# Performance work log

Measured on AMD Instinct MI355X. Metric: run time of the kernel, lower is better.

## Reference

```python
import jax, jax.numpy as jnp
import numpy as np

B, L, D, H = 2, 2048, 1024, 16
HD = D // H
ROPE_BASE = 10000.0


def _chain_info(lengths):
    """lengths: [B, L] int, chain lengths packed at the front, zeros after.
    Returns per-position within-chain positions (RoPE resets per chain),
    chain ids, and a validity mask."""
    def one(row):
        csum = jnp.cumsum(row)                      # [L]
        total = csum[-1]
        p = jnp.arange(L)
        cid = jnp.searchsorted(csum, p, side='right')  # chain id per position
        prev = jnp.where(cid > 0, csum[jnp.clip(cid - 1, 0, L - 1)], 0)
        valid = p < total
        pos = jnp.where(valid, p - prev, 0).astype(jnp.float32)
        return pos, cid, valid
    return jax.vmap(one)(lengths)


def _rope_tables(pos):
    # pos: [B, L] float -> cos/sin [B, L, 1, HD]
    inv_freq = 1.0 / (ROPE_BASE ** (jnp.arange(0, HD, 2, dtype=jnp.float32) / HD))
    freqs = pos[..., None] * inv_freq               # [B, L, HD/2]
    emb = jnp.concatenate([freqs, freqs], axis=-1)  # [B, L, HD]
    return jnp.cos(emb)[:, :, None, :], jnp.sin(emb)[:, :, None, :]


def _apply_rope(x, cos, sin):
    d = x.shape[-1]
    x1, x2 = x[..., : d // 2], x[..., d // 2:]
    return x * cos + jnp.concatenate([-x2, x1], axis=-1) * sin


def _branch(x, Wqkv, bqkv, cos, sin, allowed):
    # x: [B, L, D]; allowed: [B, L, L] bool attention mask for this branch
    qkv = x @ Wqkv.T + bqkv                          # [B, L, 3D]
    qkv = qkv.reshape(B, L, 3, H, HD)
    q, k, v = qkv[:, :, 0], qkv[:, :, 1], qkv[:, :, 2]
    q = q * (HD ** -0.5)
    q = _apply_rope(q, cos, sin)
    k = _apply_rope(k, cos, sin)
    scores = jnp.einsum('bthd,bshd->bhts', q, k)     # [B, H, L, L]
    scores = jnp.where(allowed[:, None], scores, -jnp.inf)
    probs = jax.nn.softmax(scores, axis=-1)
    probs = jnp.where(jnp.isnan(probs), 0.0, probs)  # fully-masked rows -> 0
    out = jnp.einsum('bhts,bshd->bthd', probs, v)    # [B, L, H, HD]
    return out.reshape(B, L, D)


def setup_inputs() -> dict:
    key = jax.random.key(0)
    ks = jax.random.split(key, 7)
    s = 0.02
    lens = np.zeros((B, L), np.int64)
    lens[0, :8] = [300, 250, 200, 400, 350, 248, 150, 100]   # sum 1998
    lens[1, :6] = [512, 400, 300, 360, 276, 200]             # sum 2048
    return {
        'hidden_states': jax.random.normal(ks[0], (B, L, D), jnp.float32),
        'attention_mask_in_length': jnp.asarray(lens),
        'Wqkv_intra': jax.random.normal(ks[1], (3 * D, D), jnp.float32) * s,
        'bqkv_intra': jnp.zeros((3 * D,), jnp.float32),
        'Wqkv_inter': jax.random.normal(ks[2], (3 * D, D), jnp.float32) * s,
        'bqkv_inter': jnp.zeros((3 * D,), jnp.float32),
        'Wout': jax.random.normal(ks[3], (D, D), jnp.float32) * s,
        'bout': jnp.zeros((D,), jnp.float32),
    }


def reference(hidden_states, attention_mask_in_length, Wqkv_intra, bqkv_intra,
              Wqkv_inter, bqkv_inter, Wout, bout):
    pos, cid, valid = _chain_info(attention_mask_in_length)
    cos, sin = _rope_tables(pos)
    same_chain = cid[:, :, None] == cid[:, None, :]          # [B, L, L]
    key_valid = valid[:, None, :]                            # [B, 1, L]
    allowed_intra = same_chain & key_valid
    allowed_inter = (~same_chain) & key_valid
    out_intra = _branch(hidden_states, Wqkv_intra, bqkv_intra, cos, sin, allowed_intra)
    out_inter = _branch(hidden_states, Wqkv_inter, bqkv_inter, cos, sin, allowed_inter)
    return (out_intra + out_inter) @ Wout.T + bout
```

## Files before the change

### kernel.cpp

```cpp
#include <hip/hip_runtime.h>
#include <hip/hip_bf16.h>
#include <stdint.h>

#define B 2
#define L 2048
#define D 1024
#define H 16
#define HD 64
#define NT (L / 64)
#define NQT (L / 128)
#define INVALID_CID 0x40000000
#define BHLHD ((size_t)B * H * L * HD)

typedef __hip_bfloat16 bf16;
typedef __attribute__((ext_vector_type(8))) short short8;
typedef __attribute__((ext_vector_type(4))) float floatx4;
typedef __attribute__((ext_vector_type(4))) unsigned int uint4v;

static __device__ __forceinline__ short f2bf(float f) {
    bf16 h = __float2bfloat16(f);
    return *reinterpret_cast<short*>(&h);
}

static __device__ __forceinline__ void async_copy16(const void* g, void* l) {
    __builtin_amdgcn_global_load_lds((__attribute__((address_space(1))) void*)g,
                                     (__attribute__((address_space(3))) void*)l,
                                     16, 0, 0);
}

__global__ void chain_kernel(const int* __restrict__ lens,
                             float* __restrict__ pos, int* __restrict__ cid,
                             int4* __restrict__ tinfo)
{
    __shared__ int csum[L];
    __shared__ int cids[L];
    __shared__ int part[256];
    int b = blockIdx.x;
    int t = threadIdx.x;

    int loc[8];
    int s = 0;
    #pragma unroll
    for (int j = 0; j < 8; ++j) { s += lens[b * L + t * 8 + j]; loc[j] = s; }
    part[t] = s;
    __syncthreads();
    if (t == 0) {
        int acc = 0;
        for (int i = 0; i < 256; ++i) { int v = part[i]; part[i] = acc; acc += v; }
    }
    __syncthreads();
    int base = part[t];
    #pragma unroll
    for (int j = 0; j < 8; ++j) csum[t * 8 + j] = base + loc[j];
    __syncthreads();

    int total = csum[L - 1];
    for (int p = t; p < L; p += 256) {
        int cv;
        if (p < total) {
            int lo = 0, hi = L;
            while (lo < hi) {
                int mid = (lo + hi) >> 1;
                if (csum[mid] <= p) lo = mid + 1; else hi = mid;
            }
            int prev = (lo > 0) ? csum[lo - 1] : 0;
            pos[b * L + p] = (float)(p - prev);
            cv = lo;
        } else {
            pos[b * L + p] = 0.f;
            cv = INVALID_CID;
        }
        cids[p] = cv;
        cid[b * L + p] = cv;
    }
    __syncthreads();
    if (t < NT) {
        int mn = 0x7fffffff, mx = -1, any = 0, all = 1;
        for (int j = 0; j < 64; ++j) {
            int cv = cids[t * 64 + j];
            if (cv != INVALID_CID) { any = 1; mn = min(mn, cv); mx = max(mx, cv); }
            else all = 0;
        }
        tinfo[b * NT + t] = make_int4(mn, mx, any | (all << 1), 0);
    }
}

__global__ void rope_table(const float* __restrict__ pos, float2* __restrict__ tab)
{
    int idx = blockIdx.x * 256 + threadIdx.x;
    int j = idx & 31, l = idx >> 5;
    float invf = exp2f(-(float)j * (13.287712379549449f / 32.f));
    float ang = pos[l] * invf;
    tab[idx] = make_float2(cosf(ang), sinf(ang));
}

__global__ void cast_all(const float* __restrict__ x,  const float* __restrict__ Wi,
                         const float* __restrict__ We, const float* __restrict__ Wo,
                         bf16* __restrict__ xb, bf16* __restrict__ Wib,
                         bf16* __restrict__ Web, bf16* __restrict__ Wob)
{
    int bid = blockIdx.x;
    const float* src; bf16* dst; int base;
    if      (bid < 4096)  { src = x;  dst = xb;  base = bid; }
    else if (bid < 7168)  { src = Wi; dst = Wib; base = bid - 4096; }
    else if (bid < 10240) { src = We; dst = Web; base = bid - 7168; }
    else                  { src = Wo; dst = Wob; base = bid - 10240; }
    int i = (base * 256 + threadIdx.x) * 4;
    float4 v = *(const float4*)(src + i);
    dst[i + 0] = __float2bfloat16(v.x);
    dst[i + 1] = __float2bfloat16(v.y);
    dst[i + 2] = __float2bfloat16(v.z);
    dst[i + 3] = __float2bfloat16(v.w);
}

__global__ __launch_bounds__(256, 4) void gemm_qkv(
    const bf16* __restrict__ A, const bf16* __restrict__ Bw,
    const float* __restrict__ bi, const float* __restrict__ be,
    const float2* __restrict__ tab,
    bf16* __restrict__ Qo, bf16* __restrict__ Ko, bf16* __restrict__ Vto)
{
    __shared__ short Smem[2 * 128 * 32];
    short* As = Smem;
    short* Bs = Smem + 128 * 32;

    int tid = threadIdx.x;
    int wave = tid >> 6, lane = tid & 63;
    int i15 = lane & 15, q8 = lane >> 4;
    int wm = wave & 1, wn = wave >> 1;
    int m0 = blockIdx.y * 128, n0 = blockIdx.x * 128;
    const int K = D;

    floatx4 acc[4][4];
    #pragma unroll
    for (int mt = 0; mt < 4; ++mt)
        #pragma unroll
        for (int nt = 0; nt < 4; ++nt) acc[mt][nt] = (floatx4){0.f, 0.f, 0.f, 0.f};

    const short* gA = (const short*)A  + (size_t)(m0 + wave * 32 + (lane >> 2)) * K + (lane & 3) * 8;
    const short* gB = (const short*)Bw + (size_t)(n0 + wave * 32 + (lane >> 2)) * K + (lane & 3) * 8;
    short* lA = As + wave * 1024;
    short* lB = Bs + wave * 1024;

    for (int kt = 0; kt < K; kt += 32) {
        __syncthreads();
        async_copy16(gA + kt,          lA);
        async_copy16(gA + 16 * K + kt, lA + 512);
        async_copy16(gB + kt,          lB);
        async_copy16(gB + 16 * K + kt, lB + 512);
        __syncthreads();

        short8 af[4], bfr[4];
        #pragma unroll
        for (int mt = 0; mt < 4; ++mt)
            af[mt] = *(const short8*)&As[(wm * 64 + mt * 16 + i15) * 32 + q8 * 8];
        #pragma unroll
        for (int nt = 0; nt < 4; ++nt)
            bfr[nt] = *(const short8*)&Bs[(wn * 64 + nt * 16 + i15) * 32 + q8 * 8];
        #pragma unroll
        for (int mt = 0; mt < 4; ++mt)
            #pragma unroll
            for (int nt = 0; nt < 4; ++nt)
                acc[mt][nt] = __builtin_amdgcn_mfma_f32_16x16x32_bf16(af[mt], bfr[nt], acc[mt][nt], 0, 0, 0);
    }

    int nb = n0 + wn * 64;
    int segw = nb >> 10;
    int br = (segw >= 3);
    int st = segw - 3 * br;
    int h = (nb >> 6) & (H - 1);
    int b = m0 >> 11;
    int lb = (m0 & (L - 1)) + wm * 64;

    float bv[4];
    #pragma unroll
    for (int nt = 0; nt < 4; ++nt) {
        int n = nb + nt * 16 + i15;
        bv[nt] = (n < 3 * D) ? bi[n] : be[n - 3 * D];
    }

    if (st != 2) {
        bf16* out = (st == 0 ? Qo : Ko) + (size_t)br * BHLHD;
        const size_t bh = (size_t)(b * H + h) * L;
        float qs = (st == 0) ? 0.18033688011111772f : 1.0f;
        #pragma unroll
        for (int mt = 0; mt < 4; ++mt) {
            #pragma unroll
            for (int rg = 0; rg < 4; ++rg) {
                int m = m0 + wm * 64 + mt * 16 + q8 * 4 + rg;
                int l = lb + mt * 16 + q8 * 4 + rg;
                float2 cs0 = tab[(size_t)m * 32 + i15];
                float2 cs1 = tab[(size_t)m * 32 + 16 + i15];
                size_t orow = (bh + l) * HD;
                #pragma unroll
                for (int nt = 0; nt < 4; ++nt) {
                    float x  = acc[mt][nt][rg] + bv[nt];
                    float pr = acc[mt][nt ^ 2][rg] + bv[nt ^ 2];
                    float cc = (nt & 1) ? cs1.x : cs0.x;
                    float ss = (nt & 1) ? cs1.y : cs0.y;
                    float v = qs * (x * cc + ((nt < 2) ? -pr : pr) * ss);
                    out[orow + nt * 16 + i15] = __float2bfloat16(v);
                }
            }
        }
    } else {
        bf16* out = Vto + (size_t)br * BHLHD;
        const size_t bhd = (size_t)(b * H + h) * HD;
        __syncthreads();
        short* vts = Smem + wave * 64 * 20;
        #pragma unroll
        for (int mt = 0; mt < 4; ++mt) {
            #pragma unroll
            for (int nt = 0; nt < 4; ++nt) {
                uint2 w;
                w.x = (unsigned)(unsigned short)f2bf(acc[mt][nt][0] + bv[nt]) |
                      ((unsigned)(unsigned short)f2bf(acc[mt][nt][1] + bv[nt]) << 16);
                w.y = (unsigned)(unsigned short)f2bf(acc[mt][nt][2] + bv[nt]) |
                      ((unsigned)(unsigned short)f2bf(acc[mt][nt][3] + bv[nt]) << 16);
                *(uint2*)&vts[(nt * 16 + i15) * 20 + q8 * 4] = w;
            }
            uint2 r0 = *(const uint2*)&vts[lane * 20 + 0];
            uint2 r1 = *(const uint2*)&vts[lane * 20 + 4];
            uint2 r2 = *(const uint2*)&vts[lane * 20 + 8];
            uint2 r3 = *(const uint2*)&vts[lane * 20 + 12];
            size_t ga = (bhd + lane) * L + lb + mt * 16;
            uint4v v0 = (uint4v){r0.x, r0.y, r1.x, r1.y};
            uint4v v1 = (uint4v){r2.x, r2.y, r3.x, r3.y};
            *(uint4v*)&out[ga]     = v0;
            *(uint4v*)&out[ga + 8] = v1;
        }
    }
}

__global__ __launch_bounds__(256, 4) void gemm128(
    const bf16* __restrict__ A, const bf16* __restrict__ Bw,
    const float* __restrict__ bias, void* __restrict__ Cout,
    int M, int N, int K, int c_bf16)
{
    __shared__ short As[128 * 32];
    __shared__ short Bs[128 * 32];

    int tid = threadIdx.x;
    int wave = tid >> 6, lane = tid & 63;
    int i15 = lane & 15, q8 = lane >> 4;
    int wm = wave & 1, wn = wave >> 1;
    int m0 = blockIdx.y * 128, n0 = blockIdx.x * 128;

    floatx4 acc[4][4];
    #pragma unroll
    for (int mt = 0; mt < 4; ++mt)
        #pragma unroll
        for (int nt = 0; nt < 4; ++nt) acc[mt][nt] = (floatx4){0.f, 0.f, 0.f, 0.f};

    const short* gA = (const short*)A  + (size_t)(m0 + wave * 32 + (lane >> 2)) * K + (lane & 3) * 8;
    const short* gB = (const short*)Bw + (size_t)(n0 + wave * 32 + (lane >> 2)) * K + (lane & 3) * 8;
    short* lA = As + wave * 1024;
    short* lB = Bs + wave * 1024;

    for (int kt = 0; kt < K; kt += 32) {
        __syncthreads();
        async_copy16(gA + kt,          lA);
        async_copy16(gA + 16 * K + kt, lA + 512);
        async_copy16(gB + kt,          lB);
        async_copy16(gB + 16 * K + kt, lB + 512);
        __syncthreads();

        short8 af[4], bfr[4];
        #pragma unroll
        for (int mt = 0; mt < 4; ++mt)
            af[mt] = *(const short8*)&As[(wm * 64 + mt * 16 + i15) * 32 + q8 * 8];
        #pragma unroll
        for (int nt = 0; nt < 4; ++nt)
            bfr[nt] = *(const short8*)&Bs[(wn * 64 + nt * 16 + i15) * 32 + q8 * 8];
        #pragma unroll
        for (int mt = 0; mt < 4; ++mt)
            #pragma unroll
            for (int nt = 0; nt < 4; ++nt)
                acc[mt][nt] = __builtin_amdgcn_mfma_f32_16x16x32_bf16(af[mt], bfr[nt], acc[mt][nt], 0, 0, 0);
    }

    #pragma unroll
    for (int nt = 0; nt < 4; ++nt) {
        int n = n0 + wn * 64 + nt * 16 + i15;
        float bv = bias[n];
        #pragma unroll
        for (int mt = 0; mt < 4; ++mt) {
            #pragma unroll
            for (int rg = 0; rg < 4; ++rg) {
                int m = m0 + wm * 64 + mt * 16 + q8 * 4 + rg;
                float v = acc[mt][nt][rg] + bv;
                if (c_bf16) ((bf16*)Cout)[(size_t)m * N + n] = __float2bfloat16(v);
                else        ((float*)Cout)[(size_t)m * N + n] = v;
            }
        }
    }
}

__global__ __launch_bounds__(256, 2) void attn6(
    const bf16* __restrict__ Q, const bf16* __restrict__ Kg, const bf16* __restrict__ Vtg,
    const int* __restrict__ cid, const int4* __restrict__ tinfo,
    float* __restrict__ OutF, bf16* __restrict__ OutB, const float* __restrict__ Prev,
    int branch)
{
    __shared__ short Ks[2][64][72];
    __shared__ short Vs[2][64][72];
    __shared__ int cls_s[NT];
    __shared__ int list_s[NT];
    __shared__ int nlist_s;

    int tid = threadIdx.x;
    int wave = tid >> 6, lane = tid & 63;
    int i15 = lane & 15, q8 = lane >> 4;
    int workid = ((blockIdx.x & 7) << 6) | (blockIdx.x >> 3);
    int qt = workid & (NQT - 1);
    int h  = (workid >> 4) & (H - 1);
    int b  = workid >> 8;
    int q0 = qt * 128;
    const size_t bh  = (size_t)(b * H + h) * L;
    const size_t bhd = (size_t)(b * H + h) * HD;

    short8 qf[2][2];
    int cq[2];
    #pragma unroll
    for (int g = 0; g < 2; ++g) {
        const short* qp = (const short*)Q + (bh + q0 + g * 64 + wave * 16 + i15) * HD + q8 * 8;
        qf[g][0] = *(const short8*)(qp);
        qf[g][1] = *(const short8*)(qp + 32);
        cq[g] = cid[b * L + q0 + g * 64 + wave * 16 + i15];
    }

    int4 qa = tinfo[b * NT + 2 * qt];
    int4 qb4 = tinfo[b * NT + 2 * qt + 1];
    int4 qinf;
    qinf.x = min(qa.x, qb4.x);
    qinf.y = max(qa.y, qb4.y);
    qinf.z = ((qa.z | qb4.z) & 1) | (qa.z & qb4.z & 2);
    int qall = (qinf.z >> 1) & 1;

    if (tid < NT) {
        int4 ki = tinfo[b * NT + tid];
        int kany = ki.z & 1, kall = (ki.z >> 1) & 1;
        bool disjoint = (ki.x > qinf.y) || (ki.y < qinf.x);
        bool mono = qall && kall && (qinf.x == qinf.y) && (ki.x == ki.y) && (qinf.x == ki.x);
        int cls;
        if (branch == 0) {
            if (!kany || disjoint) cls = 0;
            else if (mono) cls = 2;
            else cls = 1;
        } else {
            if (!kany || mono) cls = 0;
            else if (kall && disjoint) cls = 2;
            else cls = 1;
        }
        cls_s[tid] = cls;
    }
    __syncthreads();
    if (tid == 0) {
        int n = 0;
        for (int t = 0; t < NT; ++t) {
            int c = cls_s[t];
            if (c) list_s[n++] = (t * 64) | ((c == 2) << 16);
        }
        nlist_s = n;
    }
    __syncthreads();
    int n = nlist_s;

    int r = tid >> 2, ccol = (tid & 3) * 16;
    int sr = ((((r >> 2) & 1) | ((r >> 5) << 1)) << 4) | (((r >> 3) & 3) << 2) | (r & 3);
    const short* Kbase = (const short*)Kg  + (bh + r) * HD + ccol;
    const short* Vbase = (const short*)Vtg + (bhd + r) * L + ccol;

    int4 pk0, pk1, pv0, pv1;
    int cur = 0;
    if (n > 0) {
        cur = list_s[0];
        int kt0 = cur & 0xffff;
        pk0 = *(const int4*)(Kbase + (size_t)kt0 * HD);
        pk1 = *(const int4*)(Kbase + (size_t)kt0 * HD + 8);
        pv0 = *(const int4*)(Vbase + kt0);
        pv1 = *(const int4*)(Vbase + kt0 + 8);
    }

    floatx4 accO[2][4];
    #pragma unroll
    for (int g = 0; g < 2; ++g)
        #pragma unroll
        for (int t = 0; t < 4; ++t) accO[g][t] = (floatx4){0.f, 0.f, 0.f, 0.f};
    float lsum[2] = {0.f, 0.f};

    for (int i = 0; i < n; ++i) {
        int kt = cur & 0xffff, full = cur >> 16;
        int buf = i & 1;

        *(int4*)&Ks[buf][sr][ccol]     = pk0;
        *(int4*)&Ks[buf][sr][ccol + 8] = pk1;
        *(int4*)&Vs[buf][r][ccol]      = pv0;
        *(int4*)&Vs[buf][r][ccol + 8]  = pv1;
        __syncthreads();

        if (i + 1 < n) {
            cur = list_s[i + 1];
            int nk = cur & 0xffff;
            pk0 = *(const int4*)(Kbase + (size_t)nk * HD);
            pk1 = *(const int4*)(Kbase + (size_t)nk * HD + 8);
            pv0 = *(const int4*)(Vbase + nk);
            pv1 = *(const int4*)(Vbase + nk + 8);
        }

        unsigned int dl[2][4], dh[2][4];
        #pragma unroll
        for (int t = 0; t < 4; ++t) {
            short8 b0 = *(const short8*)&Ks[buf][t * 16 + i15][q8 * 8];
            short8 b1 = *(const short8*)&Ks[buf][t * 16 + i15][32 + q8 * 8];

            floatx4 accS[2];
            #pragma unroll
            for (int g = 0; g < 2; ++g) {
                accS[g] = (floatx4){0.f, 0.f, 0.f, 0.f};
                accS[g] = __builtin_amdgcn_mfma_f32_16x16x32_bf16(b0, qf[g][0], accS[g], 0, 0, 0);
                accS[g] = __builtin_amdgcn_mfma_f32_16x16x32_bf16(b1, qf[g][1], accS[g], 0, 0, 0);
            }

            if (!full) {
                int4 ck4 = *(const int4*)(cid + b * L + kt + (q8 << 3) + ((t & 1) << 2) + ((t >> 1) << 5));
                int ckr[4] = {ck4.x, ck4.y, ck4.z, ck4.w};
                #pragma unroll
                for (int g = 0; g < 2; ++g)
                    #pragma unroll
                    for (int rg = 0; rg < 4; ++rg) {
                        bool kv = (ckr[rg] != INVALID_CID);
                        bool match = (cq[g] == ckr[rg]);
                        bool ok = kv && (branch ? !match : match);
                        accS[g][rg] = ok ? accS[g][rg] : -1e30f;
                    }
            }

            #pragma unroll
            for (int g = 0; g < 2; ++g) {
                float p0 = __builtin_amdgcn_exp2f(accS[g][0]);
                float p1 = __builtin_amdgcn_exp2f(accS[g][1]);
                float p2 = __builtin_amdgcn_exp2f(accS[g][2]);
                float p3 = __builtin_amdgcn_exp2f(accS[g][3]);
                lsum[g] += (p0 + p1) + (p2 + p3);
                dl[g][t] = (unsigned int)(unsigned short)f2bf(p0) | ((unsigned int)(unsigned short)f2bf(p1) << 16);
                dh[g][t] = (unsigned int)(unsigned short)f2bf(p2) | ((unsigned int)(unsigned short)f2bf(p3) << 16);
            }
        }

        union { uint4v u; short8 s; } pa0[2], pa1[2];
        #pragma unroll
        for (int g = 0; g < 2; ++g) {
            pa0[g].u = (uint4v){dl[g][0], dh[g][0], dl[g][1], dh[g][1]};
            pa1[g].u = (uint4v){dl[g][2], dh[g][2], dl[g][3], dh[g][3]};
        }

        #pragma unroll
        for (int dt = 0; dt < 4; ++dt) {
            short8 vf0 = *(const short8*)&Vs[buf][dt * 16 + i15][q8 * 8];
            short8 vf1 = *(const short8*)&Vs[buf][dt * 16 + i15][32 + q8 * 8];
            #pragma unroll
            for (int g = 0; g < 2; ++g) {
                accO[g][dt] = __builtin_amdgcn_mfma_f32_16x16x32_bf16(pa0[g].s, vf0, accO[g][dt], 0, 0, 0);
                accO[g][dt] = __builtin_amdgcn_mfma_f32_16x16x32_bf16(pa1[g].s, vf1, accO[g][dt], 0, 0, 0);
            }
        }
    }

    #pragma unroll
    for (int g = 0; g < 2; ++g) {
        float ls = lsum[g];
        ls += __shfl_xor(ls, 16, 64);
        ls += __shfl_xor(ls, 32, 64);
        float inv[4];
        #pragma unroll
        for (int rg = 0; rg < 4; ++rg) {
            float lv = __shfl(ls, q8 * 4 + rg, 64);
            inv[rg] = (lv > 0.f) ? 1.f / lv : 0.f;
        }
        #pragma unroll
        for (int t = 0; t < 4; ++t) {
            #pragma unroll
            for (int rg = 0; rg < 4; ++rg) {
                size_t idx = (size_t)(b * L + q0 + g * 64 + wave * 16 + q8 * 4 + rg) * D + h * HD + t * 16 + i15;
                float o = accO[g][t][rg] * inv[rg];
                if (branch == 0) OutF[idx] = o;
                else             OutB[idx] = __float2bfloat16(o + Prev[idx]);
            }
        }
    }
}

extern "C" void kernel_launch(void* const* d_in, const int* in_sizes, int n_in,
                              void* d_out, int out_size, void* d_ws, size_t ws_size,
                              hipStream_t stream)
{
    const float* x    = (const float*)d_in[0];
    const int*   mlen = (const int*)  d_in[1];
    const float* Wi   = (const float*)d_in[2];
    const float* bi   = (const float*)d_in[3];
    const float* We   = (const float*)d_in[4];
    const float* be   = (const float*)d_in[5];
    const float* Wo   = (const float*)d_in[6];
    const float* bo   = (const float*)d_in[7];

    char* ws = (char*)d_ws;
    size_t off = 0;
    auto alloc = [&](size_t bytes) {
        void* p = ws + off;
        off += (bytes + 255) & ~(size_t)255;
        return p;
    };
    bf16*  x_b   = (bf16*) alloc((size_t)B * L * D * 2);
    bf16*  Wi_b  = (bf16*) alloc((size_t)3 * D * D * 2);
    bf16*  We_b  = (bf16*) alloc((size_t)3 * D * D * 2);
    bf16*  Wo_b  = (bf16*) alloc((size_t)D * D * 2);
    bf16*  q_b   = (bf16*) alloc(2 * BHLHD * 2);
    bf16*  k_b   = (bf16*) alloc(2 * BHLHD * 2);
    bf16*  vt_b  = (bf16*) alloc(2 * BHLHD * 2);
    float* att_i = (float*)alloc((size_t)B * L * D * 4);
    bf16*  sum_b = (bf16*) alloc((size_t)B * L * D * 2);
    float* pos   = (float*)alloc((size_t)B * L * 4);
    int*   cid   = (int*)  alloc((size_t)B * L * 4);
    int4*  tinfo = (int4*) alloc((size_t)B * NT * 16);
    float2* rtab = (float2*)alloc((size_t)B * L * 32 * 8);
    (void)ws_size; (void)n_in; (void)in_sizes; (void)out_size;

    chain_kernel<<<B, 256, 0, stream>>>(mlen, pos, cid, tinfo);
    rope_table<<<B * L * 32 / 256, 256, 0, stream>>>(pos, rtab);

    cast_all<<<11264, 256, 0, stream>>>(x, Wi, We, Wo, x_b, Wi_b, We_b, Wo_b);

    dim3 gq(6 * D / 128, B * L / 128);
    gemm_qkv<<<gq, 256, 0, stream>>>(x_b, Wi_b, bi, be, rtab, q_b, k_b, vt_b);

    attn6<<<B * H * NQT, 256, 0, stream>>>(q_b, k_b, vt_b, cid, tinfo, att_i, sum_b, att_i, 0);
    attn6<<<B * H * NQT, 256, 0, stream>>>(q_b + BHLHD, k_b + BHLHD, vt_b + BHLHD,
                                           cid, tinfo, att_i, sum_b, att_i, 1);

    dim3 go(D / 128, B * L / 128);
    gemm128<<<go, 256, 0, stream>>>(sum_b, Wo_b, bo, d_out, B * L, D, D, 0);
}
```

Baseline: 306.9 us.

## Fuse intra and inter attention branches into one kernel

Merges the two per-branch attention launches into a single kernel where each block processes both branches in sequence for the same query tile, keeping both output accumulators in registers and writing the summed bf16 result directly. This removes the fp32 intermediate buffer write and re-read and one kernel launch. The cost is doubled accumulator register pressure, which may cause spills or lower occupancy under the 2-block launch bound, and per-block work becomes longer and less balanced.

```diff
diff --git a/kernel.cpp b/kernel.cpp
--- a/kernel.cpp
+++ b/kernel.cpp
@@ -295,17 +295,16 @@
     }
 }
 
-__global__ __launch_bounds__(256, 2) void attn6(
-    const bf16* __restrict__ Q, const bf16* __restrict__ Kg, const bf16* __restrict__ Vtg,
+__global__ __launch_bounds__(256, 2) void attn7(
+    const bf16* __restrict__ Qg, const bf16* __restrict__ Kgg, const bf16* __restrict__ Vtgg,
     const int* __restrict__ cid, const int4* __restrict__ tinfo,
-    float* __restrict__ OutF, bf16* __restrict__ OutB, const float* __restrict__ Prev,
-    int branch)
+    bf16* __restrict__ Out)
 {
     __shared__ short Ks[2][64][72];
     __shared__ short Vs[2][64][72];
-    __shared__ int cls_s[NT];
-    __shared__ int list_s[NT];
-    __shared__ int nlist_s;
+    __shared__ int cls0_s[NT], cls1_s[NT];
+    __shared__ int list_s[2][NT];
+    __shared__ int nlist_s[2];
 
     int tid = threadIdx.x;
     int wave = tid >> 6, lane = tid & 63;
@@ -318,15 +317,10 @@
     const size_t bh  = (size_t)(b * H + h) * L;
     const size_t bhd = (size_t)(b * H + h) * HD;
 
-    short8 qf[2][2];
     int cq[2];
     #pragma unroll
-    for (int g = 0; g < 2; ++g) {
-        const short* qp = (const short*)Q + (bh + q0 + g * 64 + wave * 16 + i15) * HD + q8 * 8;
-        qf[g][0] = *(const short8*)(qp);
-        qf[g][1] = *(const short8*)(qp + 32);
+    for (int g = 0; g < 2; ++g)
         cq[g] = cid[b * L + q0 + g * 64 + wave * 16 + i15];
-    }
 
     int4 qa = tinfo[b * NT + 2 * qt];
     int4 qb4 = tinfo[b * NT + 2 * qt + 1];
@@ -341,153 +335,164 @@
         int kany = ki.z & 1, kall = (ki.z >> 1) & 1;
         bool disjoint = (ki.x > qinf.y) || (ki.y < qinf.x);
         bool mono = qall && kall && (qinf.x == qinf.y) && (ki.x == ki.y) && (qinf.x == ki.x);
-        int cls;
-        if (branch == 0) {
-            if (!kany || disjoint) cls = 0;
-            else if (mono) cls = 2;
-            else cls = 1;
-        } else {
-            if (!kany || mono) cls = 0;
-            else if (kall && disjoint) cls = 2;
-            else cls = 1;
-        }
-        cls_s[tid] = cls;
+        cls0_s[tid] = (!kany || disjoint) ? 0 : (mono ? 2 : 1);
+        cls1_s[tid] = (!kany || mono) ? 0 : ((kall && disjoint) ? 2 : 1);
     }
     __syncthreads();
-    if (tid == 0) {
+    if (tid < 2) {
+        const int* cls = tid ? cls1_s : cls0_s;
         int n = 0;
         for (int t = 0; t < NT; ++t) {
-            int c = cls_s[t];
-            if (c) list_s[n++] = (t * 64) | ((c == 2) << 16);
-        }
-        nlist_s = n;
+            int c = cls[t];
+            if (c) list_s[tid][n++] = (t * 64) | ((c == 2) << 16);
+        }
+        nlist_s[tid] = n;
     }
     __syncthreads();
-    int n = nlist_s;
 
     int r = tid >> 2, ccol = (tid & 3) * 16;
     int sr = ((((r >> 2) & 1) | ((r >> 5) << 1)) << 4) | (((r >> 3) & 3) << 2) | (r & 3);
-    const short* Kbase = (const short*)Kg  + (bh + r) * HD + ccol;
-    const short* Vbase = (const short*)Vtg + (bhd + r) * L + ccol;
-
-    int4 pk0, pk1, pv0, pv1;
-    int cur = 0;
-    if (n > 0) {
-        cur = list_s[0];
-        int kt0 = cur & 0xffff;
-        pk0 = *(const int4*)(Kbase + (size_t)kt0 * HD);
-        pk1 = *(const int4*)(Kbase + (size_t)kt0 * HD + 8);
-        pv0 = *(const int4*)(Vbase + kt0);
-        pv1 = *(const int4*)(Vbase + kt0 + 8);
-    }
-
-    floatx4 accO[2][4];
+
+    floatx4 accO[2][2][4];
+    #pragma unroll
+    for (int br = 0; br < 2; ++br)
+        #pragma unroll
+        for (int g = 0; g < 2; ++g)
+            #pragma unroll
+            for (int t = 0; t < 4; ++t) accO[br][g][t] = (floatx4){0.f, 0.f, 0.f, 0.f};
+    float lsum[2][2] = {{0.f, 0.f}, {0.f, 0.f}};
+
+    #pragma unroll
+    for (int br = 0; br < 2; ++br) {
+        const short* Qb    = (const short*)Qg  + (size_t)br * BHLHD;
+        const short* Kbase = (const short*)Kgg + (size_t)br * BHLHD + (bh + r) * HD + ccol;
+        const short* Vbase = (const short*)Vtgg + (size_t)br * BHLHD + (bhd + r) * L + ccol;
+        int n = nlist_s[br];
+
+        short8 qf[2][2];
+        #pragma unroll
+        for (int g = 0; g < 2; ++g) {
+            const short* qp = Qb + (bh + q0 + g * 64 + wave * 16 + i15) * HD + q8 * 8;
+            qf[g][0] = *(const short8*)(qp);
+            qf[g][1] = *(const short8*)(qp + 32);
+        }
+
+        int4 pk0, pk1, pv0, pv1;
+        int cur = 0;
+        if (n > 0) {
+            cur = list_s[br][0];
+            int kt0 = cur & 0xffff;
+            pk0 = *(const int4*)(Kbase + (size_t)kt0 * HD);
+            pk1 = *(const int4*)(Kbase + (size_t)kt0 * HD + 8);
+            pv0 = *(const int4*)(Vbase + kt0);
+            pv1 = *(const int4*)(Vbase + kt0 + 8);
+        }
+        __syncthreads();
+
+        for (int i = 0; i < n; ++i) {
+            int kt = cur & 0xffff, full = cur >> 16;
+            int buf = i & 1;
+
+            *(int4*)&Ks[buf][sr][ccol]     = pk0;
+            *(int4*)&Ks[buf][sr][ccol + 8] = pk1;
+            *(int4*)&Vs[buf][r][ccol]      = pv0;
+            *(int4*)&Vs[buf][r][ccol + 8]  = pv1;
+            __syncthreads();
+
+            if (i + 1 < n) {
+                cur = list_s[br][i + 1];
+                int nk = cur & 0xffff;
+                pk0 = *(const int4*)(Kbase + (size_t)nk * HD);
+                pk1 = *(const int4*)(Kbase + (size_t)nk * HD + 8);
+                pv0 = *(const int4*)(Vbase + nk);
+                pv1 = *(const int4*)(Vbase + nk + 8);
+            }
+
+            unsigned int dl[2][4], dh[2][4];
+            #pragma unroll
+            for (int t = 0; t < 4; ++t) {
+                short8 b0 = *(const short8*)&Ks[buf][t * 16 + i15][q8 * 8];
+                short8 b1 = *(const short8*)&Ks[buf][t * 16 + i15][32 + q8 * 8];
+
+                floatx4 accS[2];
+                #pragma unroll
+                for (int g = 0; g < 2; ++g) {
+                    accS[g] = (floatx4){0.f, 0.f, 0.f, 0.f};
+                    accS[g] = __builtin_amdgcn_mfma_f32_16x16x32_bf16(b0, qf[g][0], accS[g], 0, 0, 0);
+                    accS[g] = __builtin_amdgcn_mfma_f32_16x16x32_bf16(b1, qf[g][1], accS[g], 0, 0, 0);
+                }
+
+                if (!full) {
+                    int4 ck4 = *(const int4*)(cid + b * L + kt + (q8 << 3) + ((t & 1) << 2) + ((t >> 1) << 5));
+                    int ckr[4] = {ck4.x, ck4.y, ck4.z, ck4.w};
+                    #pragma unroll
+                    for (int g = 0; g < 2; ++g)
+                        #pragma unroll
+                        for (int rg = 0; rg < 4; ++rg) {
+                            bool kv = (ckr[rg] != INVALID_CID);
+                            bool match = (cq[g] == ckr[rg]);
+                            bool ok = kv && (br ? !match : match);
+                            accS[g][rg] = ok ? accS[g][rg] : -1e30f;
+                        }
+                }
+
+                #pragma unroll
+                for (int g = 0; g < 2; ++g) {
+                    float p0 = __builtin_amdgcn_exp2f(accS[g][0]);
+                    float p1 = __builtin_amdgcn_exp2f(accS[g][1]);
+                    float p2 = __builtin_amdgcn_exp2f(accS[g][2]);
+                    float p3 = __builtin_amdgcn_exp2f(accS[g][3]);
+                    lsum[br][g] += (p0 + p1) + (p2 + p3);
+                    dl[g][t] = (unsigned)(unsigned short)f2bf(p0) | ((unsigned)(unsigned short)f2bf(p1) << 16);
+                    dh[g][t] = (unsigned)(unsigned short)f2bf(p2) | ((unsigned)(unsigned short)f2bf(p3) << 16);
+                }
+            }
+
+            union { uint4v u; short8 s; } pa0[2], pa1[2];
+            #pragma unroll
+            for (int g = 0; g < 2; ++g) {
+                pa0[g].u = (uint4v){dl[g][0], dh[g][0], dl[g][1], dh[g][1]};
+                pa1[g].u = (uint4v){dl[g][2], dh[g][2], dl[g][3], dh[g][3]};
+            }
+
+            #pragma unroll
+            for (int dt = 0; dt < 4; ++dt) {
+                short8 vf0 = *(const short8*)&Vs[buf][dt * 16 + i15][q8 * 8];
+                short8 vf1 = *(const short8*)&Vs[buf][dt * 16 + i15][32 + q8 * 8];
+                #pragma unroll
+                for (int g = 0; g < 2; ++g) {
+                    accO[br][g][dt] = __builtin_amdgcn_mfma_f32_16x16x32_bf16(pa0[g].s, vf0, accO[br][g][dt], 0, 0, 0);
+                    accO[br][g][dt] = __builtin_amdgcn_mfma_f32_16x16x32_bf16(pa1[g].s, vf1, accO[br][g][dt], 0, 0, 0);
+                }
+            }
+        }
+    }
+
+    float inv[2][2][4];
+    #pragma unroll
+    for (int br = 0; br < 2; ++br)
+        #pragma unroll
+        for (int g = 0; g < 2; ++g) {
+            float ls = lsum[br][g];
+            ls += __shfl_xor(ls, 16, 64);
+            ls += __shfl_xor(ls, 32, 64);
+            #pragma unroll
+            for (int rg = 0; rg < 4; ++rg) {
+                float lv = __shfl(ls, q8 * 4 + rg, 64);
+                inv[br][g][rg] = (lv > 0.f) ? 1.f / lv : 0.f;
+            }
+        }
+
     #pragma unroll
     for (int g = 0; g < 2; ++g)
         #pragma unroll
-        for (int t = 0; t < 4; ++t) accO[g][t] = (floatx4){0.f, 0.f, 0.f, 0.f};
-    float lsum[2] = {0.f, 0.f};
-
-    for (int i = 0; i < n; ++i) {
-        int kt = cur & 0xffff, full = cur >> 16;
-        int buf = i & 1;
-
-        *(int4*)&Ks[buf][sr][ccol]     = pk0;
-        *(int4*)&Ks[buf][sr][ccol + 8] = pk1;
-        *(int4*)&Vs[buf][r][ccol]      = pv0;
-        *(int4*)&Vs[buf][r][ccol + 8]  = pv1;
-        __syncthreads();
-
-        if (i + 1 < n) {
-            cur = list_s[i + 1];
-            int nk = cur & 0xffff;
-            pk0 = *(const int4*)(Kbase + (size_t)nk * HD);
-            pk1 = *(const int4*)(Kbase + (size_t)nk * HD + 8);
-            pv0 = *(const int4*)(Vbase + nk);
-            pv1 = *(const int4*)(Vbase + nk + 8);
-        }
-
-        unsigned int dl[2][4], dh[2][4];
-        #pragma unroll
-        for (int t = 0; t < 4; ++t) {
-            short8 b0 = *(const short8*)&Ks[buf][t * 16 + i15][q8 * 8];
-            short8 b1 = *(const short8*)&Ks[buf][t * 16 + i15][32 + q8 * 8];
-
-            floatx4 accS[2];
-            #pragma unroll
-            for (int g = 0; g < 2; ++g) {
-                accS[g] = (floatx4){0.f, 0.f, 0.f, 0.f};
-                accS[g] = __builtin_amdgcn_mfma_f32_16x16x32_bf16(b0, qf[g][0], accS[g], 0, 0, 0);
-                accS[g] = __builtin_amdgcn_mfma_f32_16x16x32_bf16(b1, qf[g][1], accS[g], 0, 0, 0);
-            }
-
-            if (!full) {
-                int4 ck4 = *(const int4*)(cid + b * L + kt + (q8 << 3) + ((t & 1) << 2) + ((t >> 1) << 5));
-                int ckr[4] = {ck4.x, ck4.y, ck4.z, ck4.w};
-                #pragma unroll
-                for (int g = 0; g < 2; ++g)
-                    #pragma unroll
-                    for (int rg = 0; rg < 4; ++rg) {
-                        bool kv = (ckr[rg] != INVALID_CID);
-                        bool match = (cq[g] == ckr[rg]);
-                        bool ok = kv && (branch ? !match : match);
-                        accS[g][rg] = ok ? accS[g][rg] : -1e30f;
-                    }
-            }
-
-            #pragma unroll
-            for (int g = 0; g < 2; ++g) {
-                float p0 = __builtin_amdgcn_exp2f(accS[g][0]);
-                float p1 = __builtin_amdgcn_exp2f(accS[g][1]);
-                float p2 = __builtin_amdgcn_exp2f(accS[g][2]);
-                float p3 = __builtin_amdgcn_exp2f(accS[g][3]);
-                lsum[g] += (p0 + p1) + (p2 + p3);
-                dl[g][t] = (unsigned int)(unsigned short)f2bf(p0) | ((unsigned int)(unsigned short)f2bf(p1) << 16);
-                dh[g][t] = (unsigned int)(unsigned short)f2bf(p2) | ((unsigned int)(unsigned short)f2bf(p3) << 16);
-            }
-        }
-
-        union { uint4v u; short8 s; } pa0[2], pa1[2];
-        #pragma unroll
-        for (int g = 0; g < 2; ++g) {
-            pa0[g].u = (uint4v){dl[g][0], dh[g][0], dl[g][1], dh[g][1]};
-            pa1[g].u = (uint4v){dl[g][2], dh[g][2], dl[g][3], dh[g][3]};
-        }
-
-        #pragma unroll
-        for (int dt = 0; dt < 4; ++dt) {
-            short8 vf0 = *(const short8*)&Vs[buf][dt * 16 + i15][q8 * 8];
-            short8 vf1 = *(const short8*)&Vs[buf][dt * 16 + i15][32 + q8 * 8];
-            #pragma unroll
-            for (int g = 0; g < 2; ++g) {
-                accO[g][dt] = __builtin_amdgcn_mfma_f32_16x16x32_bf16(pa0[g].s, vf0, accO[g][dt], 0, 0, 0);
-                accO[g][dt] = __builtin_amdgcn_mfma_f32_16x16x32_bf16(pa1[g].s, vf1, accO[g][dt], 0, 0, 0);
-            }
-        }
-    }
-
-    #pragma unroll
-    for (int g = 0; g < 2; ++g) {
-        float ls = lsum[g];
-        ls += __shfl_xor(ls, 16, 64);
-        ls += __shfl_xor(ls, 32, 64);
-        float inv[4];
-        #pragma unroll
-        for (int rg = 0; rg < 4; ++rg) {
-            float lv = __shfl(ls, q8 * 4 + rg, 64);
-            inv[rg] = (lv > 0.f) ? 1.f / lv : 0.f;
-        }
-        #pragma unroll
-        for (int t = 0; t < 4; ++t) {
+        for (int t = 0; t < 4; ++t)
             #pragma unroll
             for (int rg = 0; rg < 4; ++rg) {
                 size_t idx = (size_t)(b * L + q0 + g * 64 + wave * 16 + q8 * 4 + rg) * D + h * HD + t * 16 + i15;
-                float o = accO[g][t][rg] * inv[rg];
-                if (branch == 0) OutF[idx] = o;
-                else             OutB[idx] = __float2bfloat16(o + Prev[idx]);
-            }
-        }
-    }
+                float o = accO[0][g][t][rg] * inv[0][g][rg] + accO[1][g][t][rg] * inv[1][g][rg];
+                Out[idx] = __float2bfloat16(o);
+            }
 }
 
 extern "C" void kernel_launch(void* const* d_in, const int* in_sizes, int n_in,
@@ -517,7 +522,6 @@
     bf16*  q_b   = (bf16*) alloc(2 * BHLHD * 2);
     bf16*  k_b   = (bf16*) alloc(2 * BHLHD * 2);
     bf16*  vt_b  = (bf16*) alloc(2 * BHLHD * 2);
-    float* att_i = (float*)alloc((size_t)B * L * D * 4);
     bf16*  sum_b = (bf16*) alloc((size_t)B * L * D * 2);
     float* pos   = (float*)alloc((size_t)B * L * 4);
     int*   cid   = (int*)  alloc((size_t)B * L * 4);
@@ -533,9 +537,7 @@
     dim3 gq(6 * D / 128, B * L / 128);
     gemm_qkv<<<gq, 256, 0, stream>>>(x_b, Wi_b, bi, be, rtab, q_b, k_b, vt_b);
 
-    attn6<<<B * H * NQT, 256, 0, stream>>>(q_b, k_b, vt_b, cid, tinfo, att_i, sum_b, att_i, 0);
-    attn6<<<B * H * NQT, 256, 0, stream>>>(q_b + BHLHD, k_b + BHLHD, vt_b + BHLHD,
-                                           cid, tinfo, att_i, sum_b, att_i, 1);
+    attn7<<<B * H * NQT, 256, 0, stream>>>(q_b, k_b, vt_b, cid, tinfo, sum_b);
 
     dim3 go(D / 128, B * L / 128);
     gemm128<<<go, 256, 0, stream>>>(sum_b, Wo_b, bo, d_out, B * L, D, D, 0);
```

Measured after the change: 290.1 us. -5.5%, faster.
